# Performance work log

Measured on AMD Instinct MI355X. Metric: run time of the kernel, lower is better.

The kernel has to match this reference:

```python
import jax, jax.numpy as jnp
import numpy as np

N_NODES = 100000
N_EDGES = 1250000
FEAT = 64
HID = 10
MOD = 10.0


def setup_inputs() -> dict:
    key = jax.random.key(0)
    ks = jax.random.split(key, 12)
    inp = {
        "X": jax.random.normal(ks[0], (N_NODES, FEAT), dtype=jnp.float32),
        "W2_0": jax.random.normal(ks[1], (2 * FEAT, HID), dtype=jnp.float32) * 0.1,
        "W1_0": jax.random.normal(ks[2], (HID, HID), dtype=jnp.float32) * 0.3,
        "W2_1": jax.random.normal(ks[3], (2 * HID, HID), dtype=jnp.float32) * 0.3,
        "W1_1": jax.random.normal(ks[4], (HID, HID), dtype=jnp.float32) * 0.3,
        "W2_2": jax.random.normal(ks[5], (2 * HID, HID), dtype=jnp.float32) * 0.3,
        "W1_2": jax.random.normal(ks[6], (HID, HID), dtype=jnp.float32) * 0.3,
        "Wf1": jax.random.normal(ks[7], (HID, FEAT), dtype=jnp.float32) * 0.3,
        "Wf2": jax.random.normal(ks[8], (FEAT, FEAT), dtype=jnp.float32) * 0.1,
        "edge_src": jax.random.randint(ks[9], (N_EDGES,), 0, N_NODES, dtype=jnp.int64 if jax.config.jax_enable_x64 else jnp.int32),
        "edge_dst": jax.random.randint(ks[10], (N_EDGES,), 0, N_NODES, dtype=jnp.int64 if jax.config.jax_enable_x64 else jnp.int32),
    }
    return inp


def _rgcn_layer(X, W2, W1, src, dst):
    # gather target (i) and source (j) node features per edge: [E, in_dim]
    X_i = X[dst]
    X_j = X[src]
    # message: dense_2(relu) then dense_1(relu), divided by mod
    m = jax.nn.relu(jnp.concatenate([X_i, X_j], axis=-1) @ W2)
    m = jax.nn.relu(m @ W1) / MOD  # [E, HID]
    # sum-aggregate messages at target nodes
    agg = jax.ops.segment_sum(m, dst, num_segments=N_NODES)
    # layer activation='relu' (identity here since messages are nonneg, kept for fidelity)
    return jax.nn.relu(agg)


def reference(X, W2_0, W1_0, W2_1, W1_1, W2_2, W1_2, Wf1, Wf2, edge_src, edge_dst):
    h = X
    for W2, W1 in ((W2_0, W1_0), (W2_1, W1_1), (W2_2, W1_2)):
        h = _rgcn_layer(h, W2, W1, edge_src, edge_dst)
    h = jax.nn.relu(h @ Wf1)
    h = jax.nn.relu(h @ Wf2)
    return h
```

## Files before the change

### kernel.cpp

```cpp
#include <hip/hip_runtime.h>

#define FEAT 64
#define HID 10
#define RS 16
#define EPB 1024
#define BSH 6
#define CHK 32

__global__ __launch_bounds__(256) void pre_l0(
    const float* __restrict__ X,
    const float* __restrict__ W2,
    float* __restrict__ A,
    float* __restrict__ B,
    int n_nodes)
{
    __shared__ float w2[128 * 10];
    for (int i = threadIdx.x; i < 1280; i += 256) w2[i] = W2[i];
    __syncthreads();

    int n = blockIdx.x * 256 + threadIdx.x;
    if (n >= n_nodes) return;

    const float4* xr = reinterpret_cast<const float4*>(X + (size_t)n * FEAT);
    float a[10], b[10];
#pragma unroll
    for (int h = 0; h < 10; h++) { a[h] = 0.f; b[h] = 0.f; }

#pragma unroll
    for (int blk = 0; blk < 16; blk++) {
        float4 u = xr[blk];
        float xv[4] = { u.x, u.y, u.z, u.w };
#pragma unroll
        for (int j = 0; j < 4; j++) {
            int k = blk * 4 + j;
#pragma unroll
            for (int h = 0; h < 10; h++) {
                a[h] = fmaf(xv[j], w2[k * 10 + h], a[h]);
                b[h] = fmaf(xv[j], w2[(64 + k) * 10 + h], b[h]);
            }
        }
    }

    float4* Ar = reinterpret_cast<float4*>(A + (size_t)n * RS);
    float4* Br = reinterpret_cast<float4*>(B + (size_t)n * RS);
    Ar[0] = make_float4(a[0], a[1], a[2], a[3]);
    Ar[1] = make_float4(a[4], a[5], a[6], a[7]);
    Ar[2] = make_float4(a[8], a[9], 0.f, 0.f);
    Br[0] = make_float4(b[0], b[1], b[2], b[3]);
    Br[1] = make_float4(b[4], b[5], b[6], b[7]);
    Br[2] = make_float4(b[8], b[9], 0.f, 0.f);
}

__global__ __launch_bounds__(256) void pre_small(
    const float* __restrict__ H,
    const float* __restrict__ W2,
    float* __restrict__ A,
    float* __restrict__ B,
    int n_nodes)
{
    __shared__ float w2[200];
    for (int i = threadIdx.x; i < 200; i += 256) w2[i] = W2[i];
    __syncthreads();

    int n = blockIdx.x * 256 + threadIdx.x;
    if (n >= n_nodes) return;

    const float4* hr = reinterpret_cast<const float4*>(H + (size_t)n * RS);
    float4 h0 = hr[0], h1 = hr[1], h2 = hr[2];
    float hv[10] = { h0.x, h0.y, h0.z, h0.w, h1.x, h1.y, h1.z, h1.w, h2.x, h2.y };

    float a[10], b[10];
#pragma unroll
    for (int h = 0; h < 10; h++) { a[h] = 0.f; b[h] = 0.f; }
#pragma unroll
    for (int k = 0; k < 10; k++) {
#pragma unroll
        for (int h = 0; h < 10; h++) {
            a[h] = fmaf(hv[k], w2[k * 10 + h], a[h]);
            b[h] = fmaf(hv[k], w2[(10 + k) * 10 + h], b[h]);
        }
    }

    float4* Ar = reinterpret_cast<float4*>(A + (size_t)n * RS);
    float4* Br = reinterpret_cast<float4*>(B + (size_t)n * RS);
    Ar[0] = make_float4(a[0], a[1], a[2], a[3]);
    Ar[1] = make_float4(a[4], a[5], a[6], a[7]);
    Ar[2] = make_float4(a[8], a[9], 0.f, 0.f);
    Br[0] = make_float4(b[0], b[1], b[2], b[3]);
    Br[1] = make_float4(b[4], b[5], b[6], b[7]);
    Br[2] = make_float4(b[8], b[9], 0.f, 0.f);
}


__global__ __launch_bounds__(256) void bin_hist_k(
    const int* __restrict__ dst, int* __restrict__ blockhist, int n_edges, int nbk)
{
    extern __shared__ int hist[];
    for (int i = threadIdx.x; i < nbk; i += 256) hist[i] = 0;
    __syncthreads();
    int base = blockIdx.x * EPB;
    for (int i = threadIdx.x; i < EPB; i += 256) {
        int e = base + i;
        if (e < n_edges) atomicAdd(&hist[dst[e] >> BSH], 1);
    }
    __syncthreads();
    int* row = blockhist + (size_t)blockIdx.x * nbk;
    for (int i = threadIdx.x; i < nbk; i += 256) row[i] = hist[i];
}

__global__ __launch_bounds__(256) void colchunk_sum_k(
    const int* __restrict__ blockhist, int* __restrict__ chunksum,
    int nbk, int nblk)
{
    int b = blockIdx.x * 256 + threadIdx.x;
    int c = blockIdx.y;
    if (b >= nbk) return;
    int k0 = c * CHK;
    int k1 = min(k0 + CHK, nblk);
    int s = 0;
    for (int k = k0; k < k1; k++) s += blockhist[(size_t)k * nbk + b];
    chunksum[(size_t)c * nbk + b] = s;
}

__global__ __launch_bounds__(256) void chunk_scan_k(
    int* __restrict__ chunksum, int* __restrict__ btot, int nbk, int nchk)
{
    int b = blockIdx.x * 256 + threadIdx.x;
    if (b >= nbk) return;
    int run = 0;
    for (int c = 0; c < nchk; c++) {
        size_t idx = (size_t)c * nbk + b;
        int v = chunksum[idx];
        chunksum[idx] = run;
        run += v;
    }
    btot[b] = run;
}

__global__ __launch_bounds__(256) void scan_k(
    const int* __restrict__ btot, int* __restrict__ bbase,
    int* __restrict__ bucket_start, int* __restrict__ start,
    int nbk, int n_nodes, int n_edges)
{
    __shared__ int ts[256];
    int t = threadIdx.x;
    int v[8];
    int s = 0;
#pragma unroll
    for (int j = 0; j < 8; j++) {
        int idx = t * 8 + j;
        v[j] = (idx < nbk) ? btot[idx] : 0;
        s += v[j];
    }
    ts[t] = s;
    __syncthreads();
    for (int off = 1; off < 256; off <<= 1) {
        int x = (t >= off) ? ts[t - off] : 0;
        __syncthreads();
        ts[t] += x;
        __syncthreads();
    }
    int run = ts[t] - s;
#pragma unroll
    for (int j = 0; j < 8; j++) {
        int idx = t * 8 + j;
        if (idx < nbk) { bbase[idx] = run; bucket_start[idx] = run; }
        run += v[j];
    }
    if (t == 255) { bucket_start[nbk] = n_edges; start[n_nodes] = n_edges; }
}

__global__ __launch_bounds__(256) void col_off2_k(
    int* __restrict__ blockhist, const int* __restrict__ chunksum,
    const int* __restrict__ bbase, int nbk, int nblk)
{
    int b = blockIdx.x * 256 + threadIdx.x;
    int c = blockIdx.y;
    if (b >= nbk) return;
    int k0 = c * CHK;
    int k1 = min(k0 + CHK, nblk);
    int run = bbase[b] + chunksum[(size_t)c * nbk + b];
    for (int k = k0; k < k1; k++) {
        size_t idx = (size_t)k * nbk + b;
        int v = blockhist[idx];
        blockhist[idx] = run;
        run += v;
    }
}

__global__ __launch_bounds__(256) void bin_scatter_k(
    const int* __restrict__ src, const int* __restrict__ dst,
    const int* __restrict__ blockhist, int* __restrict__ packed,
    int n_edges, int nbk)
{
    extern __shared__ int cur[];
    const int* row = blockhist + (size_t)blockIdx.x * nbk;
    for (int i = threadIdx.x; i < nbk; i += 256) cur[i] = row[i];
    __syncthreads();
    int base = blockIdx.x * EPB;
    for (int i = threadIdx.x; i < EPB; i += 256) {
        int e = base + i;
        if (e < n_edges) {
            int d = dst[e];
            int pos = atomicAdd(&cur[d >> BSH], 1);
            packed[pos] = ((d & 63) << 17) | src[e];
        }
    }
}

__global__ __launch_bounds__(256) void csr_k(
    const int* __restrict__ packed, const int* __restrict__ bucket_start,
    int* __restrict__ nbr, int* __restrict__ start, int n_nodes)
{
    __shared__ int hist[64];
    __shared__ int excl[64];
    __shared__ int cur[64];
    int b = blockIdx.x;
    int base = bucket_start[b];
    int end  = bucket_start[b + 1];
    if (threadIdx.x < 64) hist[threadIdx.x] = 0;
    __syncthreads();
    for (int i = base + threadIdx.x; i < end; i += 256)
        atomicAdd(&hist[packed[i] >> 17], 1);
    __syncthreads();
    if (threadIdx.x == 0) {
        int r = 0;
        for (int k = 0; k < 64; k++) { excl[k] = r; r += hist[k]; }
    }
    __syncthreads();
    if (threadIdx.x < 64) {
        cur[threadIdx.x] = excl[threadIdx.x];
        int node = (b << 6) + threadIdx.x;
        if (node < n_nodes) start[node] = base + excl[threadIdx.x];
    }
    __syncthreads();
    for (int i = base + threadIdx.x; i < end; i += 256) {
        int p = packed[i];
        int pos = base + atomicAdd(&cur[p >> 17], 1);
        nbr[pos] = p & 0x1FFFF;
    }
}

__global__ __launch_bounds__(256) void gather_k(
    const float* __restrict__ A,
    const float* __restrict__ B,
    const float* __restrict__ W1,
    const int* __restrict__ start,
    const int* __restrict__ nbr,
    float* __restrict__ H,
    int n_nodes)
{
    float w1r[100];
#pragma unroll
    for (int i = 0; i < 100; i++) w1r[i] = W1[i];

    int t = blockIdx.x * 256 + threadIdx.x;
    int n = t >> 2;
    int q = t & 3;
    if (n >= n_nodes) return;

    const float4* ar = reinterpret_cast<const float4*>(A + (size_t)n * RS);
    float4 a0 = ar[0], a1 = ar[1], a2 = ar[2];
    float av[10] = { a0.x, a0.y, a0.z, a0.w, a1.x, a1.y, a1.z, a1.w, a2.x, a2.y };

    float acc[10];
#pragma unroll
    for (int h = 0; h < 10; h++) acc[h] = 0.f;

    int beg = start[n];
    int end = start[n + 1];
    for (int i = beg + q; i < end; i += 4) {
        int s = nbr[i];
        const float4* br = reinterpret_cast<const float4*>(B + (size_t)s * RS);
        float4 b0 = br[0], b1 = br[1], b2 = br[2];
        float pre[10] = { av[0] + b0.x, av[1] + b0.y, av[2] + b0.z, av[3] + b0.w,
                          av[4] + b1.x, av[5] + b1.y, av[6] + b1.z, av[7] + b1.w,
                          av[8] + b2.x, av[9] + b2.y };
#pragma unroll
        for (int j = 0; j < 10; j++) pre[j] = fmaxf(pre[j], 0.f);
#pragma unroll
        for (int h = 0; h < 10; h++) {
            float z = 0.f;
#pragma unroll
            for (int j = 0; j < 10; j++) z = fmaf(pre[j], w1r[j * 10 + h], z);
            acc[h] += fmaxf(z, 0.f);
        }
    }

#pragma unroll
    for (int h = 0; h < 10; h++) acc[h] += __shfl_xor(acc[h], 1);
#pragma unroll
    for (int h = 0; h < 10; h++) acc[h] += __shfl_xor(acc[h], 2);

    if (q == 0) {
        float4* Hr = reinterpret_cast<float4*>(H + (size_t)n * RS);
        Hr[0] = make_float4(acc[0] * 0.1f, acc[1] * 0.1f, acc[2] * 0.1f, acc[3] * 0.1f);
        Hr[1] = make_float4(acc[4] * 0.1f, acc[5] * 0.1f, acc[6] * 0.1f, acc[7] * 0.1f);
        Hr[2] = make_float4(acc[8] * 0.1f, acc[9] * 0.1f, 0.f, 0.f);
    }
}

__global__ __launch_bounds__(256) void final_k(
    const float* __restrict__ H,
    const float* __restrict__ Wf1,
    const float* __restrict__ Wf2,
    float* __restrict__ out,
    int n_nodes)
{
    __shared__ float wf1[640];
    __shared__ float wf2s[64 * 64];
    __shared__ float tT[64 * 64];

    for (int i = threadIdx.x; i < 640; i += 256) wf1[i] = Wf1[i];
    {
        const float4* w2v = reinterpret_cast<const float4*>(Wf2);
        float4* w2s = reinterpret_cast<float4*>(wf2s);
        for (int i = threadIdx.x; i < 1024; i += 256) w2s[i] = w2v[i];
    }

    int node0 = blockIdx.x * 64;

    {
        int r = threadIdx.x & 63;
        int g = threadIdx.x >> 6;
        int node = node0 + r;
        float hv[10];
        if (node < n_nodes) {
            const float4* hr = reinterpret_cast<const float4*>(H + (size_t)node * RS);
            float4 h0 = hr[0], h1 = hr[1], h2 = hr[2];
            hv[0]=h0.x; hv[1]=h0.y; hv[2]=h0.z; hv[3]=h0.w;
            hv[4]=h1.x; hv[5]=h1.y; hv[6]=h1.z; hv[7]=h1.w;
            hv[8]=h2.x; hv[9]=h2.y;
        } else {
#pragma unroll
            for (int k = 0; k < 10; k++) hv[k] = 0.f;
        }
        __syncthreads();
#pragma unroll
        for (int j = 0; j < 16; j++) {
            int c = g * 16 + j;
            float v = 0.f;
#pragma unroll
            for (int k = 0; k < 10; k++) v = fmaf(hv[k], wf1[k * 64 + c], v);
            tT[c * 64 + r] = fmaxf(v, 0.f);
        }
    }
    __syncthreads();

    int r0 = (threadIdx.x >> 4) * 4;
    int c0 = (threadIdx.x & 15) * 4;
    float acc[4][4];
#pragma unroll
    for (int i = 0; i < 4; i++)
#pragma unroll
        for (int j = 0; j < 4; j++) acc[i][j] = 0.f;

    for (int k = 0; k < 64; k++) {
        float4 a = *reinterpret_cast<const float4*>(&tT[k * 64 + r0]);
        float4 b = *reinterpret_cast<const float4*>(&wf2s[k * 64 + c0]);
        float av[4] = { a.x, a.y, a.z, a.w };
        float bv[4] = { b.x, b.y, b.z, b.w };
#pragma unroll
        for (int i = 0; i < 4; i++)
#pragma unroll
            for (int j = 0; j < 4; j++)
                acc[i][j] = fmaf(av[i], bv[j], acc[i][j]);
    }

#pragma unroll
    for (int i = 0; i < 4; i++) {
        int node = node0 + r0 + i;
        if (node < n_nodes) {
            float4 o = make_float4(fmaxf(acc[i][0], 0.f), fmaxf(acc[i][1], 0.f),
                                   fmaxf(acc[i][2], 0.f), fmaxf(acc[i][3], 0.f));
            *reinterpret_cast<float4*>(&out[(size_t)node * FEAT + c0]) = o;
        }
    }
}

extern "C" void kernel_launch(void* const* d_in, const int* in_sizes, int n_in,
                              void* d_out, int out_size, void* d_ws, size_t ws_size,
                              hipStream_t stream) {
    const float* X    = (const float*)d_in[0];
    const float* W2_0 = (const float*)d_in[1];
    const float* W1_0 = (const float*)d_in[2];
    const float* W2_1 = (const float*)d_in[3];
    const float* W1_1 = (const float*)d_in[4];
    const float* W2_2 = (const float*)d_in[5];
    const float* W1_2 = (const float*)d_in[6];
    const float* Wf1  = (const float*)d_in[7];
    const float* Wf2  = (const float*)d_in[8];
    const int* src = (const int*)d_in[9];
    const int* dst = (const int*)d_in[10];
    float* out = (float*)d_out;

    const int n_edges = in_sizes[9];
    const int n_nodes = in_sizes[0] / FEAT;

    const int nbk  = (n_nodes + 63) >> 6;
    const int nblk = (n_edges + EPB - 1) / EPB;
    const int nchk = (nblk + CHK - 1) / CHK;

    const size_t h_elems = (size_t)n_nodes * RS;
    const size_t offH   = 0;
    const size_t offA   = offH + h_elems;
    const size_t offB   = offA + h_elems;
    const size_t offNbr = offB + h_elems;
    const size_t offPk  = offNbr + (size_t)n_edges;
    const size_t offBh  = offPk + (size_t)n_edges;
    const size_t offCs  = offBh + (size_t)nblk * nbk;
    const size_t offBt  = offCs + (size_t)nchk * nbk;
    const size_t offBb  = offBt + (size_t)nbk;
    const size_t offBs  = offBb + (size_t)nbk;
    const size_t offSt  = offBs + (size_t)nbk + 1;

    float* H        = (float*)d_ws + offH;
    float* A        = (float*)d_ws + offA;
    float* B        = (float*)d_ws + offB;
    int* nbr        = (int*)d_ws + offNbr;
    int* packed     = (int*)d_ws + offPk;
    int* blockhist  = (int*)d_ws + offBh;
    int* chunksum   = (int*)d_ws + offCs;
    int* btot       = (int*)d_ws + offBt;
    int* bbase      = (int*)d_ws + offBb;
    int* bstart     = (int*)d_ws + offBs;
    int* start      = (int*)d_ws + offSt;

    const int nb = (n_nodes + 255) / 256;
    const int gb = (n_nodes * 4 + 255) / 256;
    const int fb = (n_nodes + 63) / 64;
    const int cb = (nbk + 255) / 256;
    const size_t lds_bins = (size_t)nbk * 4;

    bin_hist_k<<<nblk, 256, lds_bins, stream>>>(dst, blockhist, n_edges, nbk);
    colchunk_sum_k<<<dim3(cb, nchk), 256, 0, stream>>>(blockhist, chunksum, nbk, nblk);
    chunk_scan_k<<<cb, 256, 0, stream>>>(chunksum, btot, nbk, nchk);
    scan_k<<<1, 256, 0, stream>>>(btot, bbase, bstart, start, nbk, n_nodes, n_edges);
    col_off2_k<<<dim3(cb, nchk), 256, 0, stream>>>(blockhist, chunksum, bbase, nbk, nblk);
    bin_scatter_k<<<nblk, 256, lds_bins, stream>>>(src, dst, blockhist, packed, n_edges, nbk);
    csr_k<<<nbk, 256, 0, stream>>>(packed, bstart, nbr, start, n_nodes);

    pre_l0<<<nb, 256, 0, stream>>>(X, W2_0, A, B, n_nodes);
    gather_k<<<gb, 256, 0, stream>>>(A, B, W1_0, start, nbr, H, n_nodes);

    pre_small<<<nb, 256, 0, stream>>>(H, W2_1, A, B, n_nodes);
    gather_k<<<gb, 256, 0, stream>>>(A, B, W1_1, start, nbr, H, n_nodes);

    pre_small<<<nb, 256, 0, stream>>>(H, W2_2, A, B, n_nodes);
    gather_k<<<gb, 256, 0, stream>>>(A, B, W1_2, start, nbr, H, n_nodes);

    final_k<<<fb, 256, 0, stream>>>(H, Wf1, Wf2, out, n_nodes);
}
```

Baseline: 281.6 us.

## Fuse next-layer projection into gather, store B in bf16, packed FMA math

Drops the separate pre_small kernels by computing the next layer's A/B projections inside the gather epilogue, spread across the four lanes of each node, with ping-pong A/B buffers. Source-side B features are stored as bf16 (32 bytes per row instead of 64) to cut the random-gather traffic. The per-edge MLP now uses packed f32x2 FMA, and the chunksum layout is transposed so each thread in the scan walks contiguous memory. Storing B in bf16 loses precision in the messages.

Measured after the change: 250.0 us. 11.2% less time.

```diff
diff --git a/kernel.cpp b/kernel.cpp
--- a/kernel.cpp
+++ b/kernel.cpp
@@ -1,17 +1,47 @@
 #include <hip/hip_runtime.h>
+#include <hip/hip_bf16.h>
 
 #define FEAT 64
 #define HID 10
 #define RS 16
+#define BRS 8
 #define EPB 1024
 #define BSH 6
 #define CHK 32
+
+typedef __attribute__((ext_vector_type(2))) float f32x2;
+
+#if defined(__has_builtin)
+#if __has_builtin(__builtin_elementwise_fma)
+#define HAVE_EW_FMA 1
+#endif
+#endif
+
+__device__ __forceinline__ f32x2 pk_fma(f32x2 a, f32x2 b, f32x2 c) {
+#ifdef HAVE_EW_FMA
+    return __builtin_elementwise_fma(a, b, c);
+#else
+    f32x2 r; r.x = fmaf(a.x, b.x, c.x); r.y = fmaf(a.y, b.y, c.y); return r;
+#endif
+}
+__device__ __forceinline__ f32x2 pk_max0(f32x2 a) {
+    f32x2 r; r.x = fmaxf(a.x, 0.f); r.y = fmaxf(a.y, 0.f); return r;
+}
+__device__ __forceinline__ float bflo(unsigned int u) { return __uint_as_float(u << 16); }
+__device__ __forceinline__ float bfhi(unsigned int u) { return __uint_as_float(u & 0xffff0000u); }
+__device__ __forceinline__ unsigned int packbf2(float lo, float hi) {
+    __hip_bfloat16 l = __float2bfloat16(lo);
+    __hip_bfloat16 h = __float2bfloat16(hi);
+    unsigned short ls = *reinterpret_cast<unsigned short*>(&l);
+    unsigned short hs = *reinterpret_cast<unsigned short*>(&h);
+    return ((unsigned int)hs << 16) | ls;
+}
 
 __global__ __launch_bounds__(256) void pre_l0(
     const float* __restrict__ X,
     const float* __restrict__ W2,
     float* __restrict__ A,
-    float* __restrict__ B,
+    unsigned int* __restrict__ Bt,
     int n_nodes)
 {
     __shared__ float w2[128 * 10];
@@ -42,53 +72,15 @@
     }
 
     float4* Ar = reinterpret_cast<float4*>(A + (size_t)n * RS);
-    float4* Br = reinterpret_cast<float4*>(B + (size_t)n * RS);
     Ar[0] = make_float4(a[0], a[1], a[2], a[3]);
     Ar[1] = make_float4(a[4], a[5], a[6], a[7]);
     Ar[2] = make_float4(a[8], a[9], 0.f, 0.f);
-    Br[0] = make_float4(b[0], b[1], b[2], b[3]);
-    Br[1] = make_float4(b[4], b[5], b[6], b[7]);
-    Br[2] = make_float4(b[8], b[9], 0.f, 0.f);
-}
-
-__global__ __launch_bounds__(256) void pre_small(
-    const float* __restrict__ H,
-    const float* __restrict__ W2,
-    float* __restrict__ A,
-    float* __restrict__ B,
-    int n_nodes)
-{
-    __shared__ float w2[200];
-    for (int i = threadIdx.x; i < 200; i += 256) w2[i] = W2[i];
-    __syncthreads();
-
-    int n = blockIdx.x * 256 + threadIdx.x;
-    if (n >= n_nodes) return;
-
-    const float4* hr = reinterpret_cast<const float4*>(H + (size_t)n * RS);
-    float4 h0 = hr[0], h1 = hr[1], h2 = hr[2];
-    float hv[10] = { h0.x, h0.y, h0.z, h0.w, h1.x, h1.y, h1.z, h1.w, h2.x, h2.y };
-
-    float a[10], b[10];
-#pragma unroll
-    for (int h = 0; h < 10; h++) { a[h] = 0.f; b[h] = 0.f; }
-#pragma unroll
-    for (int k = 0; k < 10; k++) {
-#pragma unroll
-        for (int h = 0; h < 10; h++) {
-            a[h] = fmaf(hv[k], w2[k * 10 + h], a[h]);
-            b[h] = fmaf(hv[k], w2[(10 + k) * 10 + h], b[h]);
-        }
-    }
-
-    float4* Ar = reinterpret_cast<float4*>(A + (size_t)n * RS);
-    float4* Br = reinterpret_cast<float4*>(B + (size_t)n * RS);
-    Ar[0] = make_float4(a[0], a[1], a[2], a[3]);
-    Ar[1] = make_float4(a[4], a[5], a[6], a[7]);
-    Ar[2] = make_float4(a[8], a[9], 0.f, 0.f);
-    Br[0] = make_float4(b[0], b[1], b[2], b[3]);
-    Br[1] = make_float4(b[4], b[5], b[6], b[7]);
-    Br[2] = make_float4(b[8], b[9], 0.f, 0.f);
+    unsigned int bp[5];
+#pragma unroll
+    for (int j = 0; j < 5; j++) bp[j] = packbf2(b[2 * j], b[2 * j + 1]);
+    uint4* Br = reinterpret_cast<uint4*>(Bt + (size_t)n * BRS);
+    Br[0] = make_uint4(bp[0], bp[1], bp[2], bp[3]);
+    Bt[(size_t)n * BRS + 4] = bp[4];
 }
 
 
@@ -110,7 +102,7 @@
 
 __global__ __launch_bounds__(256) void colchunk_sum_k(
     const int* __restrict__ blockhist, int* __restrict__ chunksum,
-    int nbk, int nblk)
+    int nbk, int nblk, int nchk)
 {
     int b = blockIdx.x * 256 + threadIdx.x;
     int c = blockIdx.y;
@@ -119,7 +111,7 @@
     int k1 = min(k0 + CHK, nblk);
     int s = 0;
     for (int k = k0; k < k1; k++) s += blockhist[(size_t)k * nbk + b];
-    chunksum[(size_t)c * nbk + b] = s;
+    chunksum[(size_t)b * nchk + c] = s;
 }
 
 __global__ __launch_bounds__(256) void chunk_scan_k(
@@ -128,10 +120,10 @@
     int b = blockIdx.x * 256 + threadIdx.x;
     if (b >= nbk) return;
     int run = 0;
+    int* row = chunksum + (size_t)b * nchk;
     for (int c = 0; c < nchk; c++) {
-        size_t idx = (size_t)c * nbk + b;
-        int v = chunksum[idx];
-        chunksum[idx] = run;
+        int v = row[c];
+        row[c] = run;
         run += v;
     }
     btot[b] = run;
@@ -172,14 +164,14 @@
 
 __global__ __launch_bounds__(256) void col_off2_k(
     int* __restrict__ blockhist, const int* __restrict__ chunksum,
-    const int* __restrict__ bbase, int nbk, int nblk)
+    const int* __restrict__ bbase, int nbk, int nblk, int nchk)
 {
     int b = blockIdx.x * 256 + threadIdx.x;
     int c = blockIdx.y;
     if (b >= nbk) return;
     int k0 = c * CHK;
     int k1 = min(k0 + CHK, nblk);
-    int run = bbase[b] + chunksum[(size_t)c * nbk + b];
+    int run = bbase[b] + chunksum[(size_t)b * nchk + c];
     for (int k = k0; k < k1; k++) {
         size_t idx = (size_t)k * nbk + b;
         int v = blockhist[idx];
@@ -241,18 +233,31 @@
     }
 }
 
+template<bool LAST>
 __global__ __launch_bounds__(256) void gather_k(
     const float* __restrict__ A,
-    const float* __restrict__ B,
+    const unsigned int* __restrict__ Bt,
     const float* __restrict__ W1,
+    const float* __restrict__ W2n,
     const int* __restrict__ start,
     const int* __restrict__ nbr,
-    float* __restrict__ H,
+    float* __restrict__ An,
+    unsigned int* __restrict__ Bn,
+    float* __restrict__ Hout,
     int n_nodes)
 {
-    float w1r[100];
-#pragma unroll
-    for (int i = 0; i < 100; i++) w1r[i] = W1[i];
+    __shared__ float w2s[200];
+    if (!LAST) {
+        for (int i = threadIdx.x; i < 200; i += 256) w2s[i] = W2n[i];
+        __syncthreads();
+    }
+
+    f32x2 w1p[10][5];
+#pragma unroll
+    for (int j = 0; j < 10; j++)
+#pragma unroll
+        for (int h2 = 0; h2 < 5; h2++)
+            w1p[j][h2] = (f32x2){ W1[j * 10 + 2 * h2], W1[j * 10 + 2 * h2 + 1] };
 
     int t = blockIdx.x * 256 + threadIdx.x;
     int n = t >> 2;
@@ -261,42 +266,110 @@
 
     const float4* ar = reinterpret_cast<const float4*>(A + (size_t)n * RS);
     float4 a0 = ar[0], a1 = ar[1], a2 = ar[2];
-    float av[10] = { a0.x, a0.y, a0.z, a0.w, a1.x, a1.y, a1.z, a1.w, a2.x, a2.y };
-
-    float acc[10];
-#pragma unroll
-    for (int h = 0; h < 10; h++) acc[h] = 0.f;
+    f32x2 av2[5] = { {a0.x,a0.y}, {a0.z,a0.w}, {a1.x,a1.y}, {a1.z,a1.w}, {a2.x,a2.y} };
+
+    f32x2 acc2[5];
+#pragma unroll
+    for (int h2 = 0; h2 < 5; h2++) acc2[h2] = (f32x2){0.f, 0.f};
 
     int beg = start[n];
     int end = start[n + 1];
     for (int i = beg + q; i < end; i += 4) {
         int s = nbr[i];
-        const float4* br = reinterpret_cast<const float4*>(B + (size_t)s * RS);
-        float4 b0 = br[0], b1 = br[1], b2 = br[2];
-        float pre[10] = { av[0] + b0.x, av[1] + b0.y, av[2] + b0.z, av[3] + b0.w,
-                          av[4] + b1.x, av[5] + b1.y, av[6] + b1.z, av[7] + b1.w,
-                          av[8] + b2.x, av[9] + b2.y };
-#pragma unroll
-        for (int j = 0; j < 10; j++) pre[j] = fmaxf(pre[j], 0.f);
-#pragma unroll
-        for (int h = 0; h < 10; h++) {
-            float z = 0.f;
-#pragma unroll
-            for (int j = 0; j < 10; j++) z = fmaf(pre[j], w1r[j * 10 + h], z);
-            acc[h] += fmaxf(z, 0.f);
-        }
-    }
-
-#pragma unroll
-    for (int h = 0; h < 10; h++) acc[h] += __shfl_xor(acc[h], 1);
-#pragma unroll
-    for (int h = 0; h < 10; h++) acc[h] += __shfl_xor(acc[h], 2);
-
-    if (q == 0) {
-        float4* Hr = reinterpret_cast<float4*>(H + (size_t)n * RS);
-        Hr[0] = make_float4(acc[0] * 0.1f, acc[1] * 0.1f, acc[2] * 0.1f, acc[3] * 0.1f);
-        Hr[1] = make_float4(acc[4] * 0.1f, acc[5] * 0.1f, acc[6] * 0.1f, acc[7] * 0.1f);
-        Hr[2] = make_float4(acc[8] * 0.1f, acc[9] * 0.1f, 0.f, 0.f);
+        const uint4* bp = reinterpret_cast<const uint4*>(Bt + (size_t)s * BRS);
+        uint4 u = bp[0];
+        unsigned int u4 = Bt[(size_t)s * BRS + 4];
+        f32x2 pre[5];
+        pre[0] = av2[0] + (f32x2){ bflo(u.x), bfhi(u.x) };
+        pre[1] = av2[1] + (f32x2){ bflo(u.y), bfhi(u.y) };
+        pre[2] = av2[2] + (f32x2){ bflo(u.z), bfhi(u.z) };
+        pre[3] = av2[3] + (f32x2){ bflo(u.w), bfhi(u.w) };
+        pre[4] = av2[4] + (f32x2){ bflo(u4),  bfhi(u4)  };
+#pragma unroll
+        for (int k = 0; k < 5; k++) pre[k] = pk_max0(pre[k]);
+
+        f32x2 z[5];
+#pragma unroll
+        for (int h2 = 0; h2 < 5; h2++) z[h2] = (f32x2){0.f, 0.f};
+#pragma unroll
+        for (int j2 = 0; j2 < 5; j2++) {
+            f32x2 pa = (f32x2){ pre[j2].x, pre[j2].x };
+            f32x2 pb = (f32x2){ pre[j2].y, pre[j2].y };
+#pragma unroll
+            for (int h2 = 0; h2 < 5; h2++) {
+                z[h2] = pk_fma(pa, w1p[2 * j2][h2], z[h2]);
+                z[h2] = pk_fma(pb, w1p[2 * j2 + 1][h2], z[h2]);
+            }
+        }
+#pragma unroll
+        for (int h2 = 0; h2 < 5; h2++) acc2[h2] += pk_max0(z[h2]);
+    }
+
+#pragma unroll
+    for (int h2 = 0; h2 < 5; h2++) {
+        acc2[h2].x += __shfl_xor(acc2[h2].x, 1);
+        acc2[h2].y += __shfl_xor(acc2[h2].y, 1);
+    }
+#pragma unroll
+    for (int h2 = 0; h2 < 5; h2++) {
+        acc2[h2].x += __shfl_xor(acc2[h2].x, 2);
+        acc2[h2].y += __shfl_xor(acc2[h2].y, 2);
+    }
+
+    float hv[10];
+#pragma unroll
+    for (int h2 = 0; h2 < 5; h2++) {
+        hv[2 * h2]     = acc2[h2].x * 0.1f;
+        hv[2 * h2 + 1] = acc2[h2].y * 0.1f;
+    }
+
+    if (LAST) {
+        float* Hr = Hout + (size_t)n * RS;
+        if (q == 0)      *reinterpret_cast<float4*>(Hr)     = make_float4(hv[0], hv[1], hv[2], hv[3]);
+        else if (q == 1) *reinterpret_cast<float4*>(Hr + 4) = make_float4(hv[4], hv[5], hv[6], hv[7]);
+        else if (q == 2) *reinterpret_cast<float2*>(Hr + 8) = make_float2(hv[8], hv[9]);
+    } else {
+        if (q == 0) {
+            float a[8];
+#pragma unroll
+            for (int h = 0; h < 8; h++) {
+                float zz = 0.f;
+#pragma unroll
+                for (int k = 0; k < 10; k++) zz = fmaf(hv[k], w2s[k * 10 + h], zz);
+                a[h] = zz;
+            }
+            float4* Ar = reinterpret_cast<float4*>(An + (size_t)n * RS);
+            Ar[0] = make_float4(a[0], a[1], a[2], a[3]);
+            Ar[1] = make_float4(a[4], a[5], a[6], a[7]);
+        } else if (q == 1) {
+            float a8 = 0.f, a9 = 0.f;
+#pragma unroll
+            for (int k = 0; k < 10; k++) {
+                a8 = fmaf(hv[k], w2s[k * 10 + 8], a8);
+                a9 = fmaf(hv[k], w2s[k * 10 + 9], a9);
+            }
+            *reinterpret_cast<float2*>(An + (size_t)n * RS + 8) = make_float2(a8, a9);
+        } else if (q == 2) {
+            float b[8];
+#pragma unroll
+            for (int h = 0; h < 8; h++) {
+                float zz = 0.f;
+#pragma unroll
+                for (int k = 0; k < 10; k++) zz = fmaf(hv[k], w2s[100 + k * 10 + h], zz);
+                b[h] = zz;
+            }
+            *reinterpret_cast<uint4*>(Bn + (size_t)n * BRS) =
+                make_uint4(packbf2(b[0], b[1]), packbf2(b[2], b[3]),
+                           packbf2(b[4], b[5]), packbf2(b[6], b[7]));
+        } else {
+            float b8 = 0.f, b9 = 0.f;
+#pragma unroll
+            for (int k = 0; k < 10; k++) {
+                b8 = fmaf(hv[k], w2s[100 + k * 10 + 8], b8);
+                b9 = fmaf(hv[k], w2s[100 + k * 10 + 9], b9);
+            }
+            Bn[(size_t)n * BRS + 4] = packbf2(b8, b9);
+        }
     }
 }
 
@@ -327,7 +400,8 @@
         float hv[10];
         if (node < n_nodes) {
             const float4* hr = reinterpret_cast<const float4*>(H + (size_t)node * RS);
-            float4 h0 = hr[0], h1 = hr[1], h2 = hr[2];
+            float4 h0 = hr[0], h1 = hr[1];
+            float2 h2 = *reinterpret_cast<const float2*>(H + (size_t)node * RS + 8);
             hv[0]=h0.x; hv[1]=h0.y; hv[2]=h0.z; hv[3]=h0.w;
             hv[4]=h1.x; hv[5]=h1.y; hv[6]=h1.z; hv[7]=h1.w;
             hv[8]=h2.x; hv[9]=h2.y;
@@ -402,29 +476,34 @@
     const int nchk = (nblk + CHK - 1) / CHK;
 
     const size_t h_elems = (size_t)n_nodes * RS;
+    const size_t b_elems = (size_t)n_nodes * BRS;
     const size_t offH   = 0;
-    const size_t offA   = offH + h_elems;
-    const size_t offB   = offA + h_elems;
-    const size_t offNbr = offB + h_elems;
+    const size_t offA0  = offH  + h_elems;
+    const size_t offA1  = offA0 + h_elems;
+    const size_t offB0  = offA1 + h_elems;
+    const size_t offB1  = offB0 + b_elems;
+    const size_t offNbr = offB1 + b_elems;
     const size_t offPk  = offNbr + (size_t)n_edges;
     const size_t offBh  = offPk + (size_t)n_edges;
     const size_t offCs  = offBh + (size_t)nblk * nbk;
-    const size_t offBt  = offCs + (size_t)nchk * nbk;
+    const size_t offBt  = offCs + (size_t)nbk * nchk;
     const size_t offBb  = offBt + (size_t)nbk;
     const size_t offBs  = offBb + (size_t)nbk;
     const size_t offSt  = offBs + (size_t)nbk + 1;
 
-    float* H        = (float*)d_ws + offH;
-    float* A        = (float*)d_ws + offA;
-    float* B        = (float*)d_ws + offB;
-    int* nbr        = (int*)d_ws + offNbr;
-    int* packed     = (int*)d_ws + offPk;
-    int* blockhist  = (int*)d_ws + offBh;
-    int* chunksum   = (int*)d_ws + offCs;
-    int* btot       = (int*)d_ws + offBt;
-    int* bbase      = (int*)d_ws + offBb;
-    int* bstart     = (int*)d_ws + offBs;
-    int* start      = (int*)d_ws + offSt;
+    float* H            = (float*)d_ws + offH;
+    float* A0           = (float*)d_ws + offA0;
+    float* A1           = (float*)d_ws + offA1;
+    unsigned int* B0    = (unsigned int*)d_ws + offB0;
+    unsigned int* B1    = (unsigned int*)d_ws + offB1;
+    int* nbr            = (int*)d_ws + offNbr;
+    int* packed         = (int*)d_ws + offPk;
+    int* blockhist      = (int*)d_ws + offBh;
+    int* chunksum       = (int*)d_ws + offCs;
+    int* btot           = (int*)d_ws + offBt;
+    int* bbase          = (int*)d_ws + offBb;
+    int* bstart         = (int*)d_ws + offBs;
+    int* start          = (int*)d_ws + offSt;
 
     const int nb = (n_nodes + 255) / 256;
     const int gb = (n_nodes * 4 + 255) / 256;
@@ -433,21 +512,20 @@
     const size_t lds_bins = (size_t)nbk * 4;
 
     bin_hist_k<<<nblk, 256, lds_bins, stream>>>(dst, blockhist, n_edges, nbk);
-    colchunk_sum_k<<<dim3(cb, nchk), 256, 0, stream>>>(blockhist, chunksum, nbk, nblk);
+    colchunk_sum_k<<<dim3(cb, nchk), 256, 0, stream>>>(blockhist, chunksum, nbk, nblk, nchk);
     chunk_scan_k<<<cb, 256, 0, stream>>>(chunksum, btot, nbk, nchk);
     scan_k<<<1, 256, 0, stream>>>(btot, bbase, bstart, start, nbk, n_nodes, n_edges);
-    col_off2_k<<<dim3(cb, nchk), 256, 0, stream>>>(blockhist, chunksum, bbase, nbk, nblk);
+    col_off2_k<<<dim3(cb, nchk), 256, 0, stream>>>(blockhist, chunksum, bbase, nbk, nblk, nchk);
     bin_scatter_k<<<nblk, 256, lds_bins, stream>>>(src, dst, blockhist, packed, n_edges, nbk);
     csr_k<<<nbk, 256, 0, stream>>>(packed, bstart, nbr, start, n_nodes);
 
-    pre_l0<<<nb, 256, 0, stream>>>(X, W2_0, A, B, n_nodes);
-    gather_k<<<gb, 256, 0, stream>>>(A, B, W1_0, start, nbr, H, n_nodes);
-
-    pre_small<<<nb, 256, 0, stream>>>(H, W2_1, A, B, n_nodes);
-    gather_k<<<gb, 256, 0, stream>>>(A, B, W1_1, start, nbr, H, n_nodes);
-
-    pre_small<<<nb, 256, 0, stream>>>(H, W2_2, A, B, n_nodes);
-    gather_k<<<gb, 256, 0, stream>>>(A, B, W1_2, start, nbr, H, n_nodes);
+    pre_l0<<<nb, 256, 0, stream>>>(X, W2_0, A0, B0, n_nodes);
+    gather_k<false><<<gb, 256, 0, stream>>>(A0, B0, W1_0, W2_1, start, nbr,
+                                            A1, B1, nullptr, n_nodes);
+    gather_k<false><<<gb, 256, 0, stream>>>(A1, B1, W1_1, W2_2, start, nbr,
+                                            A0, B0, nullptr, n_nodes);
+    gather_k<true><<<gb, 256, 0, stream>>>(A0, B0, W1_2, nullptr, start, nbr,
+                                           nullptr, nullptr, H, n_nodes);
 
     final_k<<<fb, 256, 0, stream>>>(H, Wf1, Wf2, out, n_nodes);
 }
```
